# Performance work log

Measured on AMD Instinct MI355X. Metric: run time of the kernel, lower is better.

Reference implementation:

```python
import jax, jax.numpy as jnp
import numpy as np

B, S, D, H, O, E = 2, 2048, 1024, 2048, 1024, 8


def setup_inputs() -> dict:
    key = jax.random.key(0)
    k_x, k_rw, k_w1, k_w3, k_w2 = jax.random.split(key, 5)
    sD = 1.0 / np.sqrt(D)
    sH = 1.0 / np.sqrt(H)
    return {
        "x": jax.random.normal(k_x, (B, S, D), dtype=jnp.float32),
        "router_w": jax.random.normal(k_rw, (E, D), dtype=jnp.float32) * sD,  # nn.Linear(D, E).weight
        "router_b": jnp.zeros((E,), dtype=jnp.float32),
        "W1": jax.random.normal(k_w1, (E, D, H), dtype=jnp.float32) * sD,  # per-expert w1 (x @ W1)
        "W3": jax.random.normal(k_w3, (E, D, H), dtype=jnp.float32) * sD,  # per-expert gate w3
        "W2": jax.random.normal(k_w2, (E, H, O), dtype=jnp.float32) * sH,  # per-expert down-proj
        "top_k": 2,
    }


def reference(x, router_w, router_b, W1, W3, W2, top_k):
    b, s, d = x.shape
    xf = x.reshape(-1, d)  # [T, D], T = B*S
    T = xf.shape[0]

    # Router: softmax over experts, then top-k and renormalize
    logits = xf @ router_w.T + router_b            # [T, E]
    probs = jax.nn.softmax(logits, axis=-1)
    top_p, top_i = jax.lax.top_k(probs, top_k)     # [T, k]
    top_p = top_p / top_p.sum(axis=-1, keepdims=True)

    # Dense all-expert SwiGLU MLPs (faithful to reference: every expert on every token)
    h = jnp.einsum('td,edh->eth', xf, W1)          # [E, T, H]
    g = jnp.einsum('td,edh->eth', xf, W3)          # [E, T, H]
    eo = jnp.einsum('eth,eho->eto', jax.nn.silu(h) * g, W2)  # [E, T, O]

    # Gather each token's top-k expert outputs and combine
    sel = eo[top_i, jnp.arange(T)[:, None]]        # [T, k, O]
    out = jnp.sum(top_p[..., None] * sel, axis=1)  # [T, O]
    return out.reshape(b, s, -1)
```

## Files before the change

### kernel.cpp

```cpp
#include <hip/hip_runtime.h>
#include <hip/hip_bf16.h>

#define TTOK 4096
#define DIM  1024
#define HID  2048
#define ODIM 1024
#define NE   8

typedef __attribute__((ext_vector_type(8))) short  short8;
typedef __attribute__((ext_vector_type(4))) float  f32x4;
typedef __attribute__((ext_vector_type(8))) unsigned short ushort8;

#define WAITVM(N) asm volatile("s_waitcnt vmcnt(" #N ")" ::: "memory")
#define BAR() __builtin_amdgcn_s_barrier()

__device__ __forceinline__ unsigned short f2bf(float f){
  unsigned u = __float_as_uint(f);
  u += 0x7fffu + ((u >> 16) & 1u);
  return (unsigned short)(u >> 16);
}

__device__ __forceinline__ void gld16(const void* g, void* l){
  __builtin_amdgcn_global_load_lds(
      (const __attribute__((address_space(1))) unsigned int*)g,
      (__attribute__((address_space(3))) unsigned int*)l, 16, 0, 0);
}

__global__ __launch_bounds__(256) void router_kernel(
    const float* __restrict__ x, const float* __restrict__ rw,
    const float* __restrict__ rb, unsigned short* __restrict__ xbf,
    int2* __restrict__ toke, float2* __restrict__ tokw)
{
  int tok  = (blockIdx.x * blockDim.x + threadIdx.x) >> 6;
  int lane = threadIdx.x & 63;
  const float4* xr = (const float4*)(x + (size_t)tok * DIM + lane * 16);
  float xv[16];
#pragma unroll
  for (int q = 0; q < 4; q++){
    float4 v = xr[q];
    xv[q*4+0]=v.x; xv[q*4+1]=v.y; xv[q*4+2]=v.z; xv[q*4+3]=v.w;
  }
  ushort8 u0, u1;
#pragma unroll
  for (int j = 0; j < 8; j++){ u0[j] = f2bf(xv[j]); u1[j] = f2bf(xv[8+j]); }
  ushort8* xo = (ushort8*)(xbf + (size_t)tok * DIM + lane * 16);
  xo[0] = u0; xo[1] = u1;

  float lg[NE];
#pragma unroll
  for (int e = 0; e < NE; e++){
    const float4* wr4 = (const float4*)(rw + (size_t)e * DIM + lane * 16);
    float s = 0.f;
#pragma unroll
    for (int q = 0; q < 4; q++){
      float4 wv = wr4[q];
      s += xv[q*4+0]*wv.x + xv[q*4+1]*wv.y + xv[q*4+2]*wv.z + xv[q*4+3]*wv.w;
    }
    lg[e] = s;
  }
#pragma unroll
  for (int e = 0; e < NE; e++)
    for (int s = 1; s < 64; s <<= 1) lg[e] += __shfl_xor(lg[e], s, 64);

  if (lane == 0){
#pragma unroll
    for (int e = 0; e < NE; e++) lg[e] += rb[e];
    int e0 = 0; float l0 = lg[0];
    for (int e = 1; e < NE; e++) if (lg[e] > l0){ l0 = lg[e]; e0 = e; }
    int e1 = -1; float l1 = -1e30f;
    for (int e = 0; e < NE; e++) if (e != e0 && lg[e] > l1){ l1 = lg[e]; e1 = e; }
    float w0 = 1.f / (1.f + __expf(l1 - l0));
    float w1 = 1.f / (1.f + __expf(l0 - l1));
    toke[tok] = make_int2(e0, e1);
    tokw[tok] = make_float2(w0, w1);
  }
}

__global__ __launch_bounds__(256) void plan_kernel(
    const int2* __restrict__ toke, const float2* __restrict__ tokw,
    int* __restrict__ counts, int* __restrict__ offs,
    int* __restrict__ tlist, float* __restrict__ wlist)
{
  const int e  = blockIdx.x;
  const int t  = threadIdx.x;
  const int lane = t & 63, wv = t >> 6;
  __shared__ int sh[4 * 8];
  __shared__ int tot[8];
  __shared__ int sw[4];

  int wcnt[NE];
#pragma unroll
  for (int ee = 0; ee < NE; ee++) wcnt[ee] = 0;
  for (int base = 0; base < TTOK; base += 256){
    int2 p = toke[base + t];
#pragma unroll
    for (int ee = 0; ee < NE; ee++){
      unsigned long long m = __ballot(p.x == ee || p.y == ee);
      if (lane == 0) wcnt[ee] += __popcll(m);
    }
  }
  if (lane == 0){
#pragma unroll
    for (int ee = 0; ee < NE; ee++) sh[wv * 8 + ee] = wcnt[ee];
  }
  __syncthreads();
  if (t < NE) tot[t] = sh[t] + sh[8 + t] + sh[16 + t] + sh[24 + t];
  __syncthreads();

  int my_off = 0;
#pragma unroll
  for (int ee = 0; ee < NE; ee++) if (ee < e) my_off += tot[ee];

  if (e == 0 && t < NE){
    counts[t] = tot[t];
    int o = 0;
    for (int ee = 0; ee < NE; ee++){ if (ee < t) o += tot[ee]; }
    offs[t] = o;
    if (t == 0){
      int s = 0;
      for (int ee = 0; ee < NE; ee++) s += tot[ee];
      offs[NE] = s;
    }
  }

  int running = my_off;
  for (int base = 0; base < TTOK; base += 256){
    int tokid = base + t;
    int2  p = toke[tokid];
    float2 wgt = tokw[tokid];
    bool s0 = (p.x == e), s1 = (p.y == e);
    bool flag = s0 || s1;
    unsigned long long m = __ballot(flag);
    int rank_in_wave = __popcll(m & ((lane == 0) ? 0ull : ((~0ull) >> (64 - lane))));
    if (lane == 0) sw[wv] = __popcll(m);
    __syncthreads();
    int wave_base = 0, tot4 = 0;
#pragma unroll
    for (int w2 = 0; w2 < 4; w2++){ int v = sw[w2]; tot4 += v; if (w2 < wv) wave_base += v; }
    if (flag){
      int pos = running + wave_base + rank_in_wave;
      tlist[pos] = tokid;
      wlist[pos] = s0 ? wgt.x : wgt.y;
    }
    running += tot4;
    __syncthreads();
  }
}

__global__ __launch_bounds__(256) void transpose_cvt(
    const float* __restrict__ in, unsigned short* __restrict__ out,
    int R, int C, int ilv, size_t ostride)
{
  __shared__ __align__(16) unsigned short tl[64 * 128];
  int e = blockIdx.z;
  const float* src = in + (size_t)e * R * C + (size_t)(blockIdx.y * 128) * C + blockIdx.x * 64;
  int t = threadIdx.x;
#pragma unroll
  for (int i = 0; i < 8; i++){
    int idx = i * 256 + t;
    int c = idx & 63, r0 = (idx >> 6) * 4;
    unsigned short v[4];
#pragma unroll
    for (int j = 0; j < 4; j++) v[j] = f2bf(src[(size_t)(r0 + j) * C + c]);
    unsigned long long pk = (unsigned long long)v[0] | ((unsigned long long)v[1] << 16)
      | ((unsigned long long)v[2] << 32) | ((unsigned long long)v[3] << 48);
    *(unsigned long long*)((char*)tl + c * 256 + (((r0 >> 3) ^ (c & 15)) * 16) + (r0 & 7) * 2) = pk;
  }
  __syncthreads();
#pragma unroll
  for (int i = 0; i < 4; i++){
    int idx = i * 256 + t;
    int c = idx >> 4, r0 = (idx & 15) * 8;
    ushort8 u = *(const ushort8*)((const char*)tl + c * 256 + (((r0 >> 3) ^ (c & 15)) * 16));
    int cg = blockIdx.x * 64 + c;
    int q  = (ilv < 0) ? cg : (((cg >> 4) << 5) + ilv + (cg & 15));
    *(ushort8*)(out + (size_t)e * ostride + (size_t)q * R + blockIdx.y * 128 + r0) = u;
  }
}


__global__ __launch_bounds__(512,2) void ffn1_kernel(
    const unsigned short* __restrict__ xbf,
    const unsigned short* __restrict__ wcat,
    unsigned short* __restrict__ abuf,
    const int* __restrict__ counts, const int* __restrict__ offs,
    const int* __restrict__ tlist)
{
  const int wgid = blockIdx.x;
  const int e = wgid & 7;
  const int q = wgid >> 3;
  const int ct = q & 15;
  const int ms = q >> 4;
  const int cnt = counts[e];
  const int off = offs[e];
  const int t = threadIdx.x;
  const int l = t & 63, w = t >> 6;
  const int wr = w >> 2, wc = w & 3;

  __shared__ __align__(16) unsigned short lds[2 * 32768];

  const int R0 = 32 * w + (l >> 2), R1 = R0 + 16;
  const int csrc = ((l & 3) ^ ((l >> 3) & 3)) * 16;
  const char* pB0 = (const char*)wcat + ((size_t)e * 4096 + ct * 256 + R0) * 2048 + csrc;
  const char* pB1 = (const char*)wcat + ((size_t)e * 4096 + ct * 256 + R1) * 2048 + csrc;

  const int chsw = ((l >> 4) ^ ((l >> 1) & 3)) * 8;
  int aro[8], bro[4];
#pragma unroll
  for (int mi = 0; mi < 8; mi++) aro[mi] = (wr * 128 + mi * 16 + (l & 15)) * 32 + chsw;
#pragma unroll
  for (int ni = 0; ni < 4; ni++) bro[ni] = (wc * 64 + ni * 16 + (l & 15)) * 32 + chsw;

  for (int mt = ms; mt * 256 < cnt; mt += 2){
    const int rbase = mt * 256;
    const int rows_left = cnt - rbase;
    int raa0 = R0 < rows_left ? R0 : rows_left - 1;
    int raa1 = R1 < rows_left ? R1 : rows_left - 1;
    const char* pA0 = (const char*)xbf + (size_t)tlist[off + rbase + raa0] * 2048 + csrc;
    const char* pA1 = (const char*)xbf + (size_t)tlist[off + rbase + raa1] * 2048 + csrc;

    auto STA = [&](int bs, int kt, int kk){
      char* d = (char*)lds + bs * 65536 + kk * 16384 + (2 * w) * 1024;
      int o = kt * 128 + kk * 64;
      gld16(pA0 + o, d); gld16(pA1 + o, d + 1024);
    };
    auto STB = [&](int bs, int kt, int kk){
      char* d = (char*)lds + bs * 65536 + 32768 + kk * 16384 + (2 * w) * 1024;
      int o = kt * 128 + kk * 64;
      gld16(pB0 + o, d); gld16(pB1 + o, d + 1024);
    };

    f32x4 acc[8][4];
#pragma unroll
    for (int i = 0; i < 8; i++)
#pragma unroll
      for (int jj = 0; jj < 4; jj++) acc[i][jj] = (f32x4){0.f,0.f,0.f,0.f};

    short8 a[4], b[4];
    auto LDA = [&](int bs, int kk, int mih){
      const unsigned short* L = lds + bs * 32768 + kk * 8192;
#pragma unroll
      for (int i = 0; i < 4; i++) a[i] = *(const short8*)(L + aro[mih * 4 + i]);
    };
    auto LDB = [&](int bs, int kk){
      const unsigned short* L = lds + bs * 32768 + 16384 + kk * 8192;
#pragma unroll
      for (int i = 0; i < 4; i++) b[i] = *(const short8*)(L + bro[i]);
    };
    auto MQ = [&](int mih){
      __builtin_amdgcn_s_setprio(1);
#pragma unroll
      for (int m4 = 0; m4 < 4; m4++)
#pragma unroll
        for (int ni = 0; ni < 4; ni++)
          acc[mih * 4 + m4][ni] = __builtin_amdgcn_mfma_f32_16x16x32_bf16(a[m4], b[ni], acc[mih * 4 + m4][ni], 0, 0, 0);
      __builtin_amdgcn_s_setprio(0);
    };

    const int NK = DIM / 64;
    STA(0, 0, 0); STB(0, 0, 0); STA(0, 0, 1); STB(0, 0, 1);
    WAITVM(0); BAR();

    for (int kt = 0; kt < NK - 1; ++kt){
      const int bs = kt & 1, nb = bs ^ 1;
      LDA(bs,0,0); LDB(bs,0); STA(nb,kt+1,0);            BAR(); MQ(0); BAR();
      LDA(bs,0,1);            STB(nb,kt+1,0); WAITVM(4); BAR(); MQ(1); BAR();
      LDA(bs,1,0); LDB(bs,1); STA(nb,kt+1,1);            BAR(); MQ(0); BAR();
      LDA(bs,1,1);            STB(nb,kt+1,1); WAITVM(4); BAR(); MQ(1); BAR();
    }
    {
      const int bs = (NK - 1) & 1;
      LDA(bs,0,0); LDB(bs,0);            BAR(); MQ(0); BAR();
      LDA(bs,0,1);            WAITVM(0); BAR(); MQ(1); BAR();
      LDA(bs,1,0); LDB(bs,1);            BAR(); MQ(0); BAR();
      LDA(bs,1,1);                       BAR(); MQ(1);
    }

#pragma unroll
    for (int mi = 0; mi < 8; mi++)
#pragma unroll
      for (int r = 0; r < 4; r++){
        int row_local = wr * 128 + mi * 16 + ((l >> 4) << 2) + r;
        if (row_local < rows_left){
          size_t pair = (size_t)(off + rbase + row_local);
          unsigned short* arow = abuf + pair * HID + ct * 128 + wc * 32 + (l & 15);
          float h0 = acc[mi][0][r], g0 = acc[mi][1][r];
          arow[0]  = f2bf((h0 / (1.f + __expf(-h0))) * g0);
          float h1 = acc[mi][2][r], g1 = acc[mi][3][r];
          arow[16] = f2bf((h1 / (1.f + __expf(-h1))) * g1);
        }
      }
    BAR();
  }
}

__global__ __launch_bounds__(512,2) void ffn2_kernel(
    const unsigned short* __restrict__ abuf,
    const unsigned short* __restrict__ w2t,
    float* __restrict__ dout,
    const int* __restrict__ counts, const int* __restrict__ offs,
    const int* __restrict__ tlist, const float* __restrict__ wlist)
{
  const int wgid = blockIdx.x;
  const int e = wgid & 7;
  const int q = wgid >> 3;
  const int ct = q & 3;
  const int ms = q >> 2;
  const int cnt = counts[e];
  const int off = offs[e];
  const int t = threadIdx.x;
  const int l = t & 63, w = t >> 6;
  const int wr = w >> 2, wc = w & 3;

  __shared__ __align__(16) unsigned short lds[2 * 32768];

  const int R0 = 32 * w + (l >> 2), R1 = R0 + 16;
  const int csrc = ((l & 3) ^ ((l >> 3) & 3)) * 16;
  const char* pB0 = (const char*)w2t + ((size_t)e * 1024 + ct * 256 + R0) * 4096 + csrc;
  const char* pB1 = (const char*)w2t + ((size_t)e * 1024 + ct * 256 + R1) * 4096 + csrc;

  const int chsw = ((l >> 4) ^ ((l >> 1) & 3)) * 8;
  int aro[8], bro[4];
#pragma unroll
  for (int mi = 0; mi < 8; mi++) aro[mi] = (wr * 128 + mi * 16 + (l & 15)) * 32 + chsw;
#pragma unroll
  for (int ni = 0; ni < 4; ni++) bro[ni] = (wc * 64 + ni * 16 + (l & 15)) * 32 + chsw;

  for (int mt = ms; mt * 256 < cnt; mt += 8){
    const int rbase = mt * 256;
    const int rows_left = cnt - rbase;
    int raa0 = R0 < rows_left ? R0 : rows_left - 1;
    int raa1 = R1 < rows_left ? R1 : rows_left - 1;
    const char* pA0 = (const char*)abuf + (size_t)(off + rbase + raa0) * 4096 + csrc;
    const char* pA1 = (const char*)abuf + (size_t)(off + rbase + raa1) * 4096 + csrc;

    auto STA = [&](int bs, int kt, int kk){
      char* d = (char*)lds + bs * 65536 + kk * 16384 + (2 * w) * 1024;
      int o = kt * 128 + kk * 64;
      gld16(pA0 + o, d); gld16(pA1 + o, d + 1024);
    };
    auto STB = [&](int bs, int kt, int kk){
      char* d = (char*)lds + bs * 65536 + 32768 + kk * 16384 + (2 * w) * 1024;
      int o = kt * 128 + kk * 64;
      gld16(pB0 + o, d); gld16(pB1 + o, d + 1024);
    };

    f32x4 acc[8][4];
#pragma unroll
    for (int i = 0; i < 8; i++)
#pragma unroll
      for (int jj = 0; jj < 4; jj++) acc[i][jj] = (f32x4){0.f,0.f,0.f,0.f};

    short8 a[4], b[4];
    auto LDA = [&](int bs, int kk, int mih){
      const unsigned short* L = lds + bs * 32768 + kk * 8192;
#pragma unroll
      for (int i = 0; i < 4; i++) a[i] = *(const short8*)(L + aro[mih * 4 + i]);
    };
    auto LDB = [&](int bs, int kk){
      const unsigned short* L = lds + bs * 32768 + 16384 + kk * 8192;
#pragma unroll
      for (int i = 0; i < 4; i++) b[i] = *(const short8*)(L + bro[i]);
    };
    auto MQ = [&](int mih){
      __builtin_amdgcn_s_setprio(1);
#pragma unroll
      for (int m4 = 0; m4 < 4; m4++)
#pragma unroll
        for (int ni = 0; ni < 4; ni++)
          acc[mih * 4 + m4][ni] = __builtin_amdgcn_mfma_f32_16x16x32_bf16(a[m4], b[ni], acc[mih * 4 + m4][ni], 0, 0, 0);
      __builtin_amdgcn_s_setprio(0);
    };

    const int NK = HID / 64;
    STA(0, 0, 0); STB(0, 0, 0); STA(0, 0, 1); STB(0, 0, 1);
    WAITVM(0); BAR();

    for (int kt = 0; kt < NK - 1; ++kt){
      const int bs = kt & 1, nb = bs ^ 1;
      LDA(bs,0,0); LDB(bs,0); STA(nb,kt+1,0);            BAR(); MQ(0); BAR();
      LDA(bs,0,1);            STB(nb,kt+1,0); WAITVM(4); BAR(); MQ(1); BAR();
      LDA(bs,1,0); LDB(bs,1); STA(nb,kt+1,1);            BAR(); MQ(0); BAR();
      LDA(bs,1,1);            STB(nb,kt+1,1); WAITVM(4); BAR(); MQ(1); BAR();
    }
    {
      const int bs = (NK - 1) & 1;
      LDA(bs,0,0); LDB(bs,0);            BAR(); MQ(0); BAR();
      LDA(bs,0,1);            WAITVM(0); BAR(); MQ(1); BAR();
      LDA(bs,1,0); LDB(bs,1);            BAR(); MQ(0); BAR();
      LDA(bs,1,1);                       BAR(); MQ(1);
    }

#pragma unroll
    for (int mi = 0; mi < 8; mi++)
#pragma unroll
      for (int r = 0; r < 4; r++){
        int row_local = wr * 128 + mi * 16 + ((l >> 4) << 2) + r;
        if (row_local < rows_left){
          int pair = off + rbase + row_local;
          int token = tlist[pair];
          float p   = wlist[pair];
          float* orow = dout + (size_t)token * ODIM + ct * 256 + wc * 64 + (l & 15);
#pragma unroll
          for (int ni = 0; ni < 4; ni++)
            atomicAdd(orow + ni * 16, p * acc[mi][ni][r]);
        }
      }
    BAR();
  }
}

extern "C" void kernel_launch(void* const* d_in, const int* in_sizes, int n_in,
                              void* d_out, int out_size, void* d_ws, size_t ws_size,
                              hipStream_t stream)
{
  const float* x  = (const float*)d_in[0];
  const float* rw = (const float*)d_in[1];
  const float* rb = (const float*)d_in[2];
  const float* W1 = (const float*)d_in[3];
  const float* W3 = (const float*)d_in[4];
  const float* W2 = (const float*)d_in[5];

  char* ws = (char*)d_ws;
  const size_t off_ctrl = 0;
  const size_t off_toke = 256;
  const size_t off_tokw = off_toke + (size_t)TTOK * 8;
  const size_t off_tl   = off_tokw + (size_t)TTOK * 8;
  const size_t off_wl   = off_tl   + (size_t)2 * TTOK * 4;
  const size_t off_xbf  = off_wl   + (size_t)2 * TTOK * 4;
  const size_t off_wcat = off_xbf  + (size_t)TTOK * DIM * 2;
  const size_t off_w2t  = off_wcat + (size_t)NE * 2 * HID * DIM * 2;
  const size_t off_ab   = off_w2t  + (size_t)NE * ODIM * HID * 2;
  const size_t need     = off_ab   + (size_t)2 * TTOK * HID * 2;
  if (ws_size < need) return;

  int* counts = (int*)(ws + off_ctrl);
  int* offs   = (int*)(ws + off_ctrl + 64);
  int2*   toke = (int2*)  (ws + off_toke);
  float2* tokw = (float2*)(ws + off_tokw);
  int*    tl   = (int*)   (ws + off_tl);
  float*  wl   = (float*) (ws + off_wl);
  unsigned short* xbf  = (unsigned short*)(ws + off_xbf);
  unsigned short* wcat = (unsigned short*)(ws + off_wcat);
  unsigned short* w2t  = (unsigned short*)(ws + off_w2t);
  unsigned short* ab   = (unsigned short*)(ws + off_ab);

  hipMemsetAsync(d_out, 0, (size_t)out_size * sizeof(float), stream);

  router_kernel<<<TTOK / 4, 256, 0, stream>>>(x, rw, rb, xbf, toke, tokw);
  plan_kernel<<<NE, 256, 0, stream>>>(toke, tokw, counts, offs, tl, wl);

  transpose_cvt<<<dim3(HID / 64, DIM / 128, NE), 256, 0, stream>>>(W1, wcat, DIM, HID, 0,  (size_t)2 * HID * DIM);
  transpose_cvt<<<dim3(HID / 64, DIM / 128, NE), 256, 0, stream>>>(W3, wcat, DIM, HID, 16, (size_t)2 * HID * DIM);
  transpose_cvt<<<dim3(ODIM / 64, HID / 128, NE), 256, 0, stream>>>(W2, w2t, HID, ODIM, -1, (size_t)ODIM * HID);

  ffn1_kernel<<<NE * 16 * 2, 512, 0, stream>>>(xbf, wcat, ab, counts, offs, tl);
  ffn2_kernel<<<NE * 4 * 8, 512, 0, stream>>>(ab, w2t, (float*)d_out, counts, offs, tl, wl);
}
```

Baseline: 269.6 us.

## Pre-gather routed token rows and replace output atomics with slot buffers plus combine

Adds a gather kernel that copies each routed token's bf16 row into a contiguous per-pair buffer, so ffn1 loads A tiles from contiguous rows and no longer looks up tlist. ffn2 now writes weighted expert outputs with plain stores into two per-slot float buffers, reusing the wcat region since it is dead by then, instead of atomically adding into the output. A combine kernel then sums the two slots, which also removes the output memset. In exchange it adds two kernel launches and extra global traffic for the gathered rows and the slot buffers.

```diff
diff --git a/kernel.cpp b/kernel.cpp
--- a/kernel.cpp
+++ b/kernel.cpp
@@ -79,7 +79,7 @@
 __global__ __launch_bounds__(256) void plan_kernel(
     const int2* __restrict__ toke, const float2* __restrict__ tokw,
     int* __restrict__ counts, int* __restrict__ offs,
-    int* __restrict__ tlist, float* __restrict__ wlist)
+    int* __restrict__ tlist, float* __restrict__ wlist, int* __restrict__ slist)
 {
   const int e  = blockIdx.x;
   const int t  = threadIdx.x;
@@ -141,10 +141,23 @@
       int pos = running + wave_base + rank_in_wave;
       tlist[pos] = tokid;
       wlist[pos] = s0 ? wgt.x : wgt.y;
+      slist[pos] = s0 ? 0 : 1;
     }
     running += tot4;
     __syncthreads();
   }
+}
+
+__global__ __launch_bounds__(256) void gather_kernel(
+    const unsigned short* __restrict__ xbf, const int* __restrict__ tlist,
+    unsigned short* __restrict__ xg)
+{
+  int pair = blockIdx.x * 4 + (threadIdx.x >> 6);
+  int lane = threadIdx.x & 63;
+  int tok  = tlist[pair];
+  const ushort8* s = (const ushort8*)(xbf + (size_t)tok * DIM + lane * 16);
+  ushort8* d = (ushort8*)(xg + (size_t)pair * DIM + lane * 16);
+  d[0] = s[0]; d[1] = s[1];
 }
 
 __global__ __launch_bounds__(256) void transpose_cvt(
@@ -178,13 +191,11 @@
   }
 }
 
-
 __global__ __launch_bounds__(512,2) void ffn1_kernel(
-    const unsigned short* __restrict__ xbf,
+    const unsigned short* __restrict__ xg,
     const unsigned short* __restrict__ wcat,
     unsigned short* __restrict__ abuf,
-    const int* __restrict__ counts, const int* __restrict__ offs,
-    const int* __restrict__ tlist)
+    const int* __restrict__ counts, const int* __restrict__ offs)
 {
   const int wgid = blockIdx.x;
   const int e = wgid & 7;
@@ -216,8 +227,8 @@
     const int rows_left = cnt - rbase;
     int raa0 = R0 < rows_left ? R0 : rows_left - 1;
     int raa1 = R1 < rows_left ? R1 : rows_left - 1;
-    const char* pA0 = (const char*)xbf + (size_t)tlist[off + rbase + raa0] * 2048 + csrc;
-    const char* pA1 = (const char*)xbf + (size_t)tlist[off + rbase + raa1] * 2048 + csrc;
+    const char* pA0 = (const char*)xg + (size_t)(off + rbase + raa0) * 2048 + csrc;
+    const char* pA1 = (const char*)xg + (size_t)(off + rbase + raa1) * 2048 + csrc;
 
     auto STA = [&](int bs, int kt, int kk){
       char* d = (char*)lds + bs * 65536 + kk * 16384 + (2 * w) * 1024;
@@ -297,9 +308,10 @@
 __global__ __launch_bounds__(512,2) void ffn2_kernel(
     const unsigned short* __restrict__ abuf,
     const unsigned short* __restrict__ w2t,
-    float* __restrict__ dout,
+    float* __restrict__ sel,
     const int* __restrict__ counts, const int* __restrict__ offs,
-    const int* __restrict__ tlist, const float* __restrict__ wlist)
+    const int* __restrict__ tlist, const float* __restrict__ wlist,
+    const int* __restrict__ slist)
 {
   const int wgid = blockIdx.x;
   const int e = wgid & 7;
@@ -400,14 +412,24 @@
           int pair = off + rbase + row_local;
           int token = tlist[pair];
           float p   = wlist[pair];
-          float* orow = dout + (size_t)token * ODIM + ct * 256 + wc * 64 + (l & 15);
+          int s     = slist[pair];
+          float* srow = sel + ((size_t)s * TTOK + token) * ODIM + ct * 256 + wc * 64 + (l & 15);
 #pragma unroll
           for (int ni = 0; ni < 4; ni++)
-            atomicAdd(orow + ni * 16, p * acc[mi][ni][r]);
+            srow[ni * 16] = p * acc[mi][ni][r];
         }
       }
     BAR();
   }
+}
+
+__global__ __launch_bounds__(256) void combine_kernel(
+    const float4* __restrict__ s0, const float4* __restrict__ s1, float4* __restrict__ o)
+{
+  int i = blockIdx.x * 256 + threadIdx.x;
+  float4 a = s0[i], b = s1[i];
+  float4 r; r.x = a.x + b.x; r.y = a.y + b.y; r.z = a.z + b.z; r.w = a.w + b.w;
+  o[i] = r;
 }
 
 extern "C" void kernel_launch(void* const* d_in, const int* in_sizes, int n_in,
@@ -427,11 +449,13 @@
   const size_t off_tokw = off_toke + (size_t)TTOK * 8;
   const size_t off_tl   = off_tokw + (size_t)TTOK * 8;
   const size_t off_wl   = off_tl   + (size_t)2 * TTOK * 4;
-  const size_t off_xbf  = off_wl   + (size_t)2 * TTOK * 4;
+  const size_t off_sl   = off_wl   + (size_t)2 * TTOK * 4;
+  const size_t off_xbf  = off_sl   + (size_t)2 * TTOK * 4;
   const size_t off_wcat = off_xbf  + (size_t)TTOK * DIM * 2;
   const size_t off_w2t  = off_wcat + (size_t)NE * 2 * HID * DIM * 2;
   const size_t off_ab   = off_w2t  + (size_t)NE * ODIM * HID * 2;
-  const size_t need     = off_ab   + (size_t)2 * TTOK * HID * 2;
+  const size_t off_xg   = off_ab   + (size_t)2 * TTOK * HID * 2;
+  const size_t need     = off_xg   + (size_t)2 * TTOK * DIM * 2;
   if (ws_size < need) return;
 
   int* counts = (int*)(ws + off_ctrl);
@@ -440,20 +464,24 @@
   float2* tokw = (float2*)(ws + off_tokw);
   int*    tl   = (int*)   (ws + off_tl);
   float*  wl   = (float*) (ws + off_wl);
+  int*    sl   = (int*)   (ws + off_sl);
   unsigned short* xbf  = (unsigned short*)(ws + off_xbf);
   unsigned short* wcat = (unsigned short*)(ws + off_wcat);
   unsigned short* w2t  = (unsigned short*)(ws + off_w2t);
   unsigned short* ab   = (unsigned short*)(ws + off_ab);
-
-  hipMemsetAsync(d_out, 0, (size_t)out_size * sizeof(float), stream);
+  unsigned short* xg   = (unsigned short*)(ws + off_xg);
+  float* sel = (float*)(ws + off_wcat);
 
   router_kernel<<<TTOK / 4, 256, 0, stream>>>(x, rw, rb, xbf, toke, tokw);
-  plan_kernel<<<NE, 256, 0, stream>>>(toke, tokw, counts, offs, tl, wl);
+  plan_kernel<<<NE, 256, 0, stream>>>(toke, tokw, counts, offs, tl, wl, sl);
+  gather_kernel<<<2 * TTOK / 4, 256, 0, stream>>>(xbf, tl, xg);
 
   transpose_cvt<<<dim3(HID / 64, DIM / 128, NE), 256, 0, stream>>>(W1, wcat, DIM, HID, 0,  (size_t)2 * HID * DIM);
   transpose_cvt<<<dim3(HID / 64, DIM / 128, NE), 256, 0, stream>>>(W3, wcat, DIM, HID, 16, (size_t)2 * HID * DIM);
   transpose_cvt<<<dim3(ODIM / 64, HID / 128, NE), 256, 0, stream>>>(W2, w2t, HID, ODIM, -1, (size_t)ODIM * HID);
 
-  ffn1_kernel<<<NE * 16 * 2, 512, 0, stream>>>(xbf, wcat, ab, counts, offs, tl);
-  ffn2_kernel<<<NE * 4 * 8, 512, 0, stream>>>(ab, w2t, (float*)d_out, counts, offs, tl, wl);
-}
+  ffn1_kernel<<<NE * 16 * 2, 512, 0, stream>>>(xg, wcat, ab, counts, offs);
+  ffn2_kernel<<<NE * 4 * 8, 512, 0, stream>>>(ab, w2t, sel, counts, offs, tl, wl, sl);
+  combine_kernel<<<(TTOK * ODIM / 4) / 256, 256, 0, stream>>>(
+      (const float4*)sel, (const float4*)(sel + (size_t)TTOK * ODIM), (float4*)d_out);
+}
```

Measured after the change: 268.1 us. No clear change (-0.6%).
